# Kernel tuning notes

Measured on AMD Instinct MI355X. Metric: run time of the kernel, lower is better.

## Reference

```python
import jax, jax.numpy as jnp
import numpy as np

N = 16777216  # 2^24 samples


def setup_inputs() -> dict:
    key = jax.random.key(0)
    k1, k2 = jax.random.split(key)
    confidences = jax.random.uniform(k1, (N,), dtype=jnp.float32)
    accuracies = jax.random.randint(k2, (N,), 0, 2).astype(jnp.float32)
    return {"confidences": confidences, "accuracies": accuracies, "num_bins": 15}


def reference(confidences, accuracies, num_bins):
    # Bin b covers (b/num_bins, (b+1)/num_bins]; ceil(c*num_bins)-1 gives that bin.
    # Values outside (0, 1] fall in no bin (matches the torch strict/inclusive bounds)
    # and are routed to an overflow segment that is dropped.
    n = confidences.shape[0]
    idx = jnp.ceil(confidences * num_bins).astype(jnp.int32) - 1
    valid = (confidences > 0.0) & (confidences <= 1.0)
    idx = jnp.where(valid, jnp.clip(idx, 0, num_bins - 1), num_bins)
    sum_conf = jax.ops.segment_sum(confidences, idx, num_segments=num_bins + 1)[:num_bins]
    sum_acc = jax.ops.segment_sum(accuracies, idx, num_segments=num_bins + 1)[:num_bins]
    # ece = sum_b |avg_conf_b - avg_acc_b| * (cnt_b / n) = sum_b |sum_conf_b - sum_acc_b| / n
    # Empty bins have zero sums and contribute 0, matching the prop_in_bin > 0 guard.
    ece = jnp.sum(jnp.abs(sum_conf - sum_acc)) / n
    return ece
```

## Files before the change

### kernel.cpp

```cpp
#include <hip/hip_runtime.h>


#define NB 15

__global__ __launch_bounds__(256) void ece_hist(
        const float* __restrict__ conf,
        const float* __restrict__ acc,
        float* __restrict__ partials,
        int n4, int n, int nblocks) {
    float bins[NB];
#pragma unroll
    for (int b = 0; b < NB; ++b) bins[b] = 0.0f;

    const float4* __restrict__ c4 = (const float4*)conf;
    const float4* __restrict__ a4 = (const float4*)acc;
    const int stride = gridDim.x * blockDim.x;

    for (int i = blockIdx.x * blockDim.x + threadIdx.x; i < n4; i += stride) {
        float4 c = c4[i];
        float4 a = a4[i];
        float cv[4] = {c.x, c.y, c.z, c.w};
        float av[4] = {a.x, a.y, a.z, a.w};
#pragma unroll
        for (int j = 0; j < 4; ++j) {
            float v = cv[j];
            float d = v - av[j];
            int idx = (int)ceilf(v * 15.0f) - 1;
            bool valid = (v > 0.0f) && (v <= 1.0f);
            idx = valid ? idx : -1;
#pragma unroll
            for (int b = 0; b < NB; ++b)
                bins[b] += (idx == b) ? d : 0.0f;
        }
    }

    if (blockIdx.x == 0) {
        for (int i = n4 * 4 + (int)threadIdx.x; i < n; i += blockDim.x) {
            float v = conf[i];
            float d = v - acc[i];
            int idx = (int)ceilf(v * 15.0f) - 1;
            bool valid = (v > 0.0f) && (v <= 1.0f);
            idx = valid ? idx : -1;
#pragma unroll
            for (int b = 0; b < NB; ++b)
                bins[b] += (idx == b) ? d : 0.0f;
        }
    }

#pragma unroll
    for (int b = 0; b < NB; ++b) {
        float v = bins[b];
#pragma unroll
        for (int off = 32; off > 0; off >>= 1)
            v += __shfl_down(v, off, 64);
        bins[b] = v;
    }

    __shared__ float wsum[4][NB];
    const int wave = threadIdx.x >> 6;
    const int lane = threadIdx.x & 63;
    if (lane == 0) {
#pragma unroll
        for (int b = 0; b < NB; ++b) wsum[wave][b] = bins[b];
    }
    __syncthreads();

    if (threadIdx.x < NB) {
        float s = wsum[0][threadIdx.x] + wsum[1][threadIdx.x]
                + wsum[2][threadIdx.x] + wsum[3][threadIdx.x];
        partials[threadIdx.x * nblocks + blockIdx.x] = s;
    }
}

__global__ __launch_bounds__(960) void ece_final(
        const float* __restrict__ partials,
        float* __restrict__ out, int nblocks, float inv_n) {
    __shared__ float bsum[NB];
    const int wave = threadIdx.x >> 6;
    const int lane = threadIdx.x & 63;

    float s = 0.0f;
    for (int i = lane; i < nblocks; i += 64)
        s += partials[wave * nblocks + i];
#pragma unroll
    for (int off = 32; off > 0; off >>= 1)
        s += __shfl_down(s, off, 64);
    if (lane == 0) bsum[wave] = s;
    __syncthreads();

    if (threadIdx.x == 0) {
        float t = 0.0f;
#pragma unroll
        for (int b = 0; b < NB; ++b) t += fabsf(bsum[b]);
        out[0] = t * inv_n;
    }
}

extern "C" void kernel_launch(void* const* d_in, const int* in_sizes, int n_in,
                              void* d_out, int out_size, void* d_ws, size_t ws_size,
                              hipStream_t stream) {
    const float* conf = (const float*)d_in[0];
    const float* acc  = (const float*)d_in[1];
    float* partials   = (float*)d_ws;
    float* out        = (float*)d_out;

    const int n  = in_sizes[0];
    const int n4 = n / 4;

    int nblocks = 2048;
    while ((size_t)NB * nblocks * sizeof(float) > ws_size && nblocks > 1)
        nblocks >>= 1;
    int max_grid = (n4 + 255) / 256;
    if (nblocks > max_grid) nblocks = max_grid;
    if (nblocks < 1) nblocks = 1;

    ece_hist<<<nblocks, 256, 0, stream>>>(conf, acc, partials, n4, n, nblocks);
    ece_final<<<1, 960, 0, stream>>>(partials, out, nblocks, 1.0f / (float)n);
}
```

Baseline: 161.0 us.

## Use per-thread shared-memory histogram rows with LDS atomics and prefetching

```diff
diff --git a/kernel.cpp b/kernel.cpp
--- a/kernel.cpp
+++ b/kernel.cpp
@@ -2,73 +2,83 @@
 
 
 #define NB 15
+#define ROW 16
+#define BLOCK 256
 
-__global__ __launch_bounds__(256) void ece_hist(
+__global__ __launch_bounds__(BLOCK) void ece_hist(
         const float* __restrict__ conf,
         const float* __restrict__ acc,
         float* __restrict__ partials,
         int n4, int n, int nblocks) {
-    float bins[NB];
+    __shared__ float rows[BLOCK * ROW];
+    __shared__ float red[BLOCK];
+
+    const int t = threadIdx.x;
 #pragma unroll
-    for (int b = 0; b < NB; ++b) bins[b] = 0.0f;
+    for (int s = 0; s < ROW; ++s) rows[t * ROW + s] = 0.0f;
+    __syncthreads();
+
+    float* myrow = &rows[t * ROW];
 
     const float4* __restrict__ c4 = (const float4*)conf;
     const float4* __restrict__ a4 = (const float4*)acc;
     const int stride = gridDim.x * blockDim.x;
+    int i = blockIdx.x * blockDim.x + t;
 
-    for (int i = blockIdx.x * blockDim.x + threadIdx.x; i < n4; i += stride) {
-        float4 c = c4[i];
-        float4 a = a4[i];
+    float4 c, a;
+    bool have = (i < n4);
+    if (have) { c = c4[i]; a = a4[i]; }
+    while (have) {
+        const int inext = i + stride;
+        const bool hn = (inext < n4);
+        float4 cn, an;
+        if (hn) { cn = c4[inext]; an = a4[inext]; }
+
         float cv[4] = {c.x, c.y, c.z, c.w};
         float av[4] = {a.x, a.y, a.z, a.w};
 #pragma unroll
         for (int j = 0; j < 4; ++j) {
             float v = cv[j];
             float d = v - av[j];
-            int idx = (int)ceilf(v * 15.0f) - 1;
+            int b = (int)(v * 15.0f);
             bool valid = (v > 0.0f) && (v <= 1.0f);
-            idx = valid ? idx : -1;
-#pragma unroll
-            for (int b = 0; b < NB; ++b)
-                bins[b] += (idx == b) ? d : 0.0f;
+            b = valid ? b : NB;
+            int slot = (b + t) & (ROW - 1);
+            unsafeAtomicAdd(&myrow[slot], d);
         }
+        c = cn; a = an; i = inext; have = hn;
     }
 
     if (blockIdx.x == 0) {
-        for (int i = n4 * 4 + (int)threadIdx.x; i < n; i += blockDim.x) {
-            float v = conf[i];
-            float d = v - acc[i];
-            int idx = (int)ceilf(v * 15.0f) - 1;
+        for (int k = n4 * 4 + t; k < n; k += BLOCK) {
+            float v = conf[k];
+            float d = v - acc[k];
+            int b = (int)(v * 15.0f);
             bool valid = (v > 0.0f) && (v <= 1.0f);
-            idx = valid ? idx : -1;
-#pragma unroll
-            for (int b = 0; b < NB; ++b)
-                bins[b] += (idx == b) ? d : 0.0f;
+            b = valid ? b : NB;
+            unsafeAtomicAdd(&myrow[(b + t) & (ROW - 1)], d);
         }
-    }
-
-#pragma unroll
-    for (int b = 0; b < NB; ++b) {
-        float v = bins[b];
-#pragma unroll
-        for (int off = 32; off > 0; off >>= 1)
-            v += __shfl_down(v, off, 64);
-        bins[b] = v;
-    }
-
-    __shared__ float wsum[4][NB];
-    const int wave = threadIdx.x >> 6;
-    const int lane = threadIdx.x & 63;
-    if (lane == 0) {
-#pragma unroll
-        for (int b = 0; b < NB; ++b) wsum[wave][b] = bins[b];
     }
     __syncthreads();
 
-    if (threadIdx.x < NB) {
-        float s = wsum[0][threadIdx.x] + wsum[1][threadIdx.x]
-                + wsum[2][threadIdx.x] + wsum[3][threadIdx.x];
-        partials[threadIdx.x * nblocks + blockIdx.x] = s;
+    {
+        const int b = t & 15;
+        const int g = t >> 4;
+        float s = 0.0f;
+#pragma unroll
+        for (int k = 0; k < 16; ++k) {
+            const int r = g * 16 + k;
+            s += rows[r * ROW + ((b + r) & (ROW - 1))];
+        }
+        red[g * 16 + b] = s;
+    }
+    __syncthreads();
+
+    if (t < NB) {
+        float s = 0.0f;
+#pragma unroll
+        for (int g = 0; g < 16; ++g) s += red[g * 16 + t];
+        partials[t * nblocks + blockIdx.x] = s;
     }
 }
 
@@ -89,10 +99,10 @@
     __syncthreads();
 
     if (threadIdx.x == 0) {
-        float t = 0.0f;
+        float tt = 0.0f;
 #pragma unroll
-        for (int b = 0; b < NB; ++b) t += fabsf(bsum[b]);
-        out[0] = t * inv_n;
+        for (int b = 0; b < NB; ++b) tt += fabsf(bsum[b]);
+        out[0] = tt * inv_n;
     }
 }
 
@@ -110,10 +120,10 @@
     int nblocks = 2048;
     while ((size_t)NB * nblocks * sizeof(float) > ws_size && nblocks > 1)
         nblocks >>= 1;
-    int max_grid = (n4 + 255) / 256;
+    int max_grid = (n4 + BLOCK - 1) / BLOCK;
     if (nblocks > max_grid) nblocks = max_grid;
     if (nblocks < 1) nblocks = 1;
 
-    ece_hist<<<nblocks, 256, 0, stream>>>(conf, acc, partials, n4, n, nblocks);
+    ece_hist<<<nblocks, BLOCK, 0, stream>>>(conf, acc, partials, n4, n, nblocks);
     ece_final<<<1, 960, 0, stream>>>(partials, out, nblocks, 1.0f / (float)n);
 }
```

Result: slower. 204.6 us (+27.1%).
